# Performance work log

Measured on AMD Instinct MI355X. Metric: run time of the kernel, lower is better.

## Reference

```python
import jax, jax.numpy as jnp
import numpy as np

LN_EPS = 1e-5
OPM_EPS = 1e-3


def setup_inputs() -> dict:
    key = jax.random.key(0)
    ks = jax.random.split(key, 8)
    S, N, c_m, c_h, c_z = 128, 256, 256, 32, 128
    m = jax.random.normal(ks[0], (S, N, c_m), dtype=jnp.float32)
    mask = jnp.ones((S, N), dtype=jnp.float32)
    ln_w = jnp.ones((c_m,), dtype=jnp.float32)
    ln_b = jnp.zeros((c_m,), dtype=jnp.float32)
    sc1 = 1.0 / np.sqrt(c_m)
    w1 = jax.random.uniform(ks[1], (c_m, c_h), jnp.float32, -sc1, sc1)
    b1 = jax.random.uniform(ks[2], (c_h,), jnp.float32, -sc1, sc1)
    w2 = jax.random.uniform(ks[3], (c_m, c_h), jnp.float32, -sc1, sc1)
    b2 = jax.random.uniform(ks[4], (c_h,), jnp.float32, -sc1, sc1)
    sco = 1.0 / np.sqrt(c_h * c_h)
    wo = jax.random.uniform(ks[5], (c_h * c_h, c_z), jnp.float32, -sco, sco)
    bo = jax.random.uniform(ks[6], (c_z,), jnp.float32, -sco, sco)
    return {"m": m, "mask": mask, "ln_w": ln_w, "ln_b": ln_b,
            "w1": w1, "b1": b1, "w2": w2, "b2": b2, "wo": wo, "bo": bo}


def reference(m, mask, ln_w, ln_b, w1, b1, w2, b2, wo, bo):
    # LayerNorm over c_m
    mu = jnp.mean(m, axis=-1, keepdims=True)
    var = jnp.var(m, axis=-1, keepdims=True)
    ln = (m - mu) * jax.lax.rsqrt(var + LN_EPS) * ln_w + ln_b
    mk = mask[..., None]                       # [S, N, 1]
    a = (ln @ w1 + b1) * mk                    # [S, N, c_h]
    b = (ln @ w2 + b2) * mk                    # [S, N, c_h]
    # outer-product mean over the MSA dim s: [N, N, c_h, c_h]
    S, N, ch = a.shape
    outer = jnp.einsum('sic,sjd->ijcd', a, b).reshape(N, N, ch * ch)
    outer = outer @ wo + bo                    # [N, N, c_z]
    norm = jnp.einsum('si,sj->ij', mask, mask)[..., None] + OPM_EPS
    return outer / norm
```

## Files before the change

kernel.cpp:

```cpp
#include <hip/hip_runtime.h>
#include <hip/hip_bf16.h>

typedef __attribute__((ext_vector_type(8))) short short8;
typedef __attribute__((ext_vector_type(4))) short short4v;
typedef __attribute__((ext_vector_type(4))) float float4v;

#define S_DIM 128
#define N_DIM 256
#define CM    256
#define CH    32
#define CZ    128

static __device__ __forceinline__ short f2bf(float v) {
    return __builtin_bit_cast(short, __float2bfloat16(v));
}

__global__ __launch_bounds__(256) void prep_aux_kernel(
    const float* __restrict__ m, const float* __restrict__ mask,
    const float* __restrict__ lnw, const float* __restrict__ lnb,
    const float* __restrict__ w1, const float* __restrict__ b1,
    const float* __restrict__ w2, const float* __restrict__ b2,
    const float* __restrict__ wo, const float* __restrict__ bo,
    __hip_bfloat16* __restrict__ a_t, __hip_bfloat16* __restrict__ b_t,
    __hip_bfloat16* __restrict__ wo_f, float* __restrict__ ninv)
{
    __shared__ __align__(16) char lds_raw[101376];
    __hip_bfloat16* ln_lds = (__hip_bfloat16*)lds_raw;
    __hip_bfloat16* w_lds  = (__hip_bfloat16*)(lds_raw + 67584);
    __hip_bfloat16* st_lds = (__hip_bfloat16*)lds_raw;

    const int bid = blockIdx.x, t = threadIdx.x;

    if (bid >= 320) {
        int i0 = (bid - 320) * 4, j = t;
        float a0 = 0.f, a1 = 0.f, a2 = 0.f, a3 = 0.f;
        for (int s = 0; s < S_DIM; ++s) {
            float mj = mask[s * N_DIM + j];
            a0 += mask[s * N_DIM + i0 + 0] * mj;
            a1 += mask[s * N_DIM + i0 + 1] * mj;
            a2 += mask[s * N_DIM + i0 + 2] * mj;
            a3 += mask[s * N_DIM + i0 + 3] * mj;
        }
        ninv[(i0 + 0) * N_DIM + j] = 1.0f / (a0 + 1e-3f);
        ninv[(i0 + 1) * N_DIM + j] = 1.0f / (a1 + 1e-3f);
        ninv[(i0 + 2) * N_DIM + j] = 1.0f / (a2 + 1e-3f);
        ninv[(i0 + 3) * N_DIM + j] = 1.0f / (a3 + 1e-3f);
        return;
    }
    if (bid >= 256) {
        int fidx = (bid - 256) * 256 + t;
        int l  = fidx & 63;
        int d  = (fidx >> 6) & 31;
        int zt = fidx >> 11;
        int z  = zt * 16 + (l & 15);
        int cb = (l >> 4) * 8;
        short8 frag;
        #pragma unroll
        for (int j = 0; j < 8; ++j)
            frag[j] = f2bf(wo[(size_t)((cb + j) * 32 + d) * CZ + z]);
        *(short8*)&wo_f[(size_t)fidx * 8] = frag;
        return;
    }

    const int lane = t & 63, wv = t >> 6;
    const int q = lane >> 4, c16 = lane & 15;
    const int n0 = (bid & 63) * 4, s0 = (bid >> 6) * 32;

    #pragma unroll 4
    for (int i = 0; i < 64; ++i) {
        int e = i * 256 + t;
        int k = e >> 6, c = e & 63;
        float v = (c < CH) ? w1[k * CH + c] : w2[k * CH + (c - CH)];
        w_lds[c * 264 + k] = __float2bfloat16(v);
    }

    float4 lw = ((const float4*)lnw)[lane];
    float4 lb = ((const float4*)lnb)[lane];

    #pragma unroll 2
    for (int it = 0; it < 32; ++it) {
        int rl = wv * 32 + it;
        int r  = (s0 + (rl >> 2)) * N_DIM + n0 + (rl & 3);
        float4 mv = ((const float4*)(m + (size_t)r * CM))[lane];
        float s1 = mv.x + mv.y + mv.z + mv.w;
        float s2 = mv.x*mv.x + mv.y*mv.y + mv.z*mv.z + mv.w*mv.w;
        #pragma unroll
        for (int o = 32; o > 0; o >>= 1) {
            s1 += __shfl_xor(s1, o, 64);
            s2 += __shfl_xor(s2, o, 64);
        }
        float mu  = s1 * (1.0f / 256.0f);
        float var = s2 * (1.0f / 256.0f) - mu * mu;
        float rs  = rsqrtf(var + 1e-5f);
        int base = rl * 264 + lane * 4;
        ln_lds[base + 0] = __float2bfloat16((mv.x - mu) * rs * lw.x + lb.x);
        ln_lds[base + 1] = __float2bfloat16((mv.y - mu) * rs * lw.y + lb.y);
        ln_lds[base + 2] = __float2bfloat16((mv.z - mu) * rs * lw.z + lb.z);
        ln_lds[base + 3] = __float2bfloat16((mv.w - mu) * rs * lw.w + lb.w);
    }
    __syncthreads();

    float4v acc[2][4];
    #pragma unroll
    for (int rt = 0; rt < 2; ++rt)
        #pragma unroll
        for (int ct = 0; ct < 4; ++ct)
            acc[rt][ct] = (float4v){0.f, 0.f, 0.f, 0.f};
    #pragma unroll
    for (int ks = 0; ks < 8; ++ks) {
        int k0 = ks * 32 + q * 8;
        short8 af0 = *(const short8*)&ln_lds[(wv * 32      + c16) * 264 + k0];
        short8 af1 = *(const short8*)&ln_lds[(wv * 32 + 16 + c16) * 264 + k0];
        #pragma unroll
        for (int ct = 0; ct < 4; ++ct) {
            short8 wb = *(const short8*)&w_lds[(ct * 16 + c16) * 264 + k0];
            acc[0][ct] = __builtin_amdgcn_mfma_f32_16x16x32_bf16(af0, wb, acc[0][ct], 0, 0, 0);
            acc[1][ct] = __builtin_amdgcn_mfma_f32_16x16x32_bf16(af1, wb, acc[1][ct], 0, 0, 0);
        }
    }
    __syncthreads();

    #pragma unroll
    for (int rt = 0; rt < 2; ++rt) {
        int sl = wv * 8 + rt * 4 + q;
        #pragma unroll
        for (int ct = 0; ct < 4; ++ct) {
            int cc = ct * 16 + c16;
            float bias = (cc < CH) ? b1[cc] : b2[cc - CH];
            #pragma unroll
            for (int rr = 0; rr < 4; ++rr) {
                int r = (s0 + sl) * N_DIM + n0 + rr;
                float val = (acc[rt][ct][rr] + bias) * mask[r];
                st_lds[(rr * 64 + cc) * 40 + sl] = __float2bfloat16(val);
            }
        }
    }
    __syncthreads();

    {
        int nl = t >> 6, cc = t & 63;
        int colg = (n0 + nl) * CH + (cc < CH ? cc : cc - CH);
        __hip_bfloat16* dst = (cc < CH ? a_t : b_t) + (size_t)colg * S_DIM + s0;
        #pragma unroll
        for (int v = 0; v < 4; ++v)
            *(short8*)(dst + v * 8) = *(const short8*)&st_lds[t * 40 + v * 8];
    }
}

__global__ __launch_bounds__(512, 4) void main_kernel(
    const __hip_bfloat16* __restrict__ a_t, const __hip_bfloat16* __restrict__ b_t,
    const __hip_bfloat16* __restrict__ wo_f, const float* __restrict__ bo,
    const float* __restrict__ ninv, float* __restrict__ out)
{
    __shared__ __align__(16) short lds[33280];

    const int t = threadIdx.x, l = t & 63, wv = t >> 6;
    const int q = l >> 4, c16 = l & 15;
    const int bi = blockIdx.x, bj0 = blockIdx.y * 2;
    const int wr = wv & 3, wc = wv >> 2;
    const size_t Ibase = (size_t)bi * 128;

    short8 af[4][2];
    #pragma unroll
    for (int sk = 0; sk < 4; ++sk) {
        int koff = sk * 32 + q * 8;
        #pragma unroll
        for (int ti = 0; ti < 2; ++ti) {
            int row = wr * 32 + ti * 16 + c16;
            af[sk][ti] = *(const short8*)&a_t[(Ibase + row) * S_DIM + koff];
        }
    }

    #pragma unroll
    for (int tau = 0; tau < 2; ++tau) {
        const size_t Jbase = (size_t)(bj0 + tau) * 128;
        float4v acc[2][4];
        #pragma unroll
        for (int ti = 0; ti < 2; ++ti)
            #pragma unroll
            for (int tj = 0; tj < 4; ++tj)
                acc[ti][tj] = (float4v){0.f, 0.f, 0.f, 0.f};

        #pragma unroll
        for (int st = 0; st < 2; ++st) {
            #pragma unroll
            for (int i = 0; i < 2; ++i) {
                int f  = i * 8 + wv;
                int h  = f >> 3, ti = (f >> 1) & 3, kk = f & 1;
                int row  = h * 64 + ti * 16 + c16;
                int koff = st * 64 + kk * 32 + q * 8;
                *(short8*)&lds[f * 512 + l * 8] =
                    *(const short8*)&b_t[(Jbase + row) * S_DIM + koff];
            }
            __syncthreads();
            #pragma unroll
            for (int kk = 0; kk < 2; ++kk) {
                short8 bf[4];
                #pragma unroll
                for (int tj = 0; tj < 4; ++tj)
                    bf[tj] = *(const short8*)&lds[((wc * 4 + tj) * 2 + kk) * 512 + l * 8];
                #pragma unroll
                for (int ti = 0; ti < 2; ++ti)
                    #pragma unroll
                    for (int tj = 0; tj < 4; ++tj)
                        acc[ti][tj] = __builtin_amdgcn_mfma_f32_16x16x32_bf16(
                            af[st * 2 + kk][ti], bf[tj], acc[ti][tj], 0, 0, 0);
            }
            __syncthreads();
        }

        const int pb = tau ? 0 : 16640;
        #pragma unroll
        for (int ti = 0; ti < 2; ++ti)
            #pragma unroll
            for (int tj = 0; tj < 4; ++tj) {
                int d  = ((tj & 1) * 16) + c16;
                int c0 = ti * 16 + q * 4;
                int p  = wr * 4 + wc * 2 + (tj >> 1);
                short4v pk;
                #pragma unroll
                for (int rr = 0; rr < 4; ++rr)
                    pk[rr] = f2bf(acc[ti][tj][rr]);
                *(short4v*)&lds[pb + d * 520 + (c0 >> 3) * 128 + p * 8 + (c0 & 7)] = pk;
            }
    }
    __syncthreads();

    float4v oacc[2];
    oacc[0] = (float4v){0.f, 0.f, 0.f, 0.f};
    oacc[1] = (float4v){0.f, 0.f, 0.f, 0.f};
    const __hip_bfloat16* wbase = wo_f + (size_t)wv * 32 * 512;
    #pragma unroll 4
    for (int d = 0; d < 32; ++d) {
        short8 p0 = *(const short8*)&lds[16640 + d * 520 + l * 8];
        short8 p1 = *(const short8*)&lds[        d * 520 + l * 8];
        short8 wf = *(const short8*)&wbase[(size_t)(d * 512 + l * 8)];
        oacc[0] = __builtin_amdgcn_mfma_f32_16x16x32_bf16(p0, wf, oacc[0], 0, 0, 0);
        oacc[1] = __builtin_amdgcn_mfma_f32_16x16x32_bf16(p1, wf, oacc[1], 0, 0, 0);
    }

    const int gi = bi * 4 + q;
    const int z  = wv * 16 + c16;
    const float bz = bo[z];
    #pragma unroll
    for (int tau = 0; tau < 2; ++tau) {
        const int bj = bj0 + tau;
        #pragma unroll
        for (int rr = 0; rr < 4; ++rr) {
            int gj = bj * 4 + rr;
            float nv = ninv[gi * N_DIM + gj];
            out[((size_t)gi * N_DIM + gj) * CZ + z] = (oacc[tau][rr] + bz) * nv;
        }
    }
}

extern "C" void kernel_launch(void* const* d_in, const int* in_sizes, int n_in,
                              void* d_out, int out_size, void* d_ws, size_t ws_size,
                              hipStream_t stream) {
    const float* m    = (const float*)d_in[0];
    const float* mask = (const float*)d_in[1];
    const float* lnw  = (const float*)d_in[2];
    const float* lnb  = (const float*)d_in[3];
    const float* w1   = (const float*)d_in[4];
    const float* b1   = (const float*)d_in[5];
    const float* w2   = (const float*)d_in[6];
    const float* b2   = (const float*)d_in[7];
    const float* wo   = (const float*)d_in[8];
    const float* bo   = (const float*)d_in[9];
    float* out = (float*)d_out;

    char* ws = (char*)d_ws;
    __hip_bfloat16* a_t  = (__hip_bfloat16*)ws;
    __hip_bfloat16* b_t  = (__hip_bfloat16*)(ws + (2u << 20));
    __hip_bfloat16* wo_f = (__hip_bfloat16*)(ws + (4u << 20));
    float*          ninv = (float*)(ws + (4u << 20) + (256u << 10));

    prep_aux_kernel<<<384, 256, 0, stream>>>(m, mask, lnw, lnb, w1, b1, w2, b2,
                                             wo, bo, a_t, b_t, wo_f, ninv);
    main_kernel<<<dim3(64, 32), 512, 0, stream>>>(a_t, b_t, wo_f, bo, ninv, out);
}
```

Baseline: 169.3 us.

## Store a/b projections in MFMA fragment layout and prefetch wo fragments

The prep kernel now handles 2 residues per block (twice as many blocks, smaller LDS footprint) and writes the a/b projections directly in the per-lane MFMA fragment order. The main kernel can then load A and B operands as contiguous 1KB fragments instead of strided row gathers. The final wo projection loop now double-buffers wo fragments in registers to overlap global loads with MFMAs. Risks include extra register pressure in the main kernel and more, smaller prep blocks that re-stage the w1/w2 weights into LDS more often.

```diff
diff --git a/kernel.cpp b/kernel.cpp
--- a/kernel.cpp
+++ b/kernel.cpp
@@ -14,6 +14,7 @@
 static __device__ __forceinline__ short f2bf(float v) {
     return __builtin_bit_cast(short, __float2bfloat16(v));
 }
+
 
 __global__ __launch_bounds__(256) void prep_aux_kernel(
     const float* __restrict__ m, const float* __restrict__ mask,
@@ -21,18 +22,18 @@
     const float* __restrict__ w1, const float* __restrict__ b1,
     const float* __restrict__ w2, const float* __restrict__ b2,
     const float* __restrict__ wo, const float* __restrict__ bo,
-    __hip_bfloat16* __restrict__ a_t, __hip_bfloat16* __restrict__ b_t,
+    __hip_bfloat16* __restrict__ a_f, __hip_bfloat16* __restrict__ b_f,
     __hip_bfloat16* __restrict__ wo_f, float* __restrict__ ninv)
 {
-    __shared__ __align__(16) char lds_raw[101376];
+    __shared__ __align__(16) char lds_raw[77824];
     __hip_bfloat16* ln_lds = (__hip_bfloat16*)lds_raw;
-    __hip_bfloat16* w_lds  = (__hip_bfloat16*)(lds_raw + 67584);
-    __hip_bfloat16* st_lds = (__hip_bfloat16*)lds_raw;
+    __hip_bfloat16* w_lds  = (__hip_bfloat16*)(lds_raw + 33792);
+    __hip_bfloat16* st_lds = (__hip_bfloat16*)(lds_raw + 67584);
 
     const int bid = blockIdx.x, t = threadIdx.x;
 
-    if (bid >= 320) {
-        int i0 = (bid - 320) * 4, j = t;
+    if (bid >= 576) {
+        int i0 = (bid - 576) * 4, j = t;
         float a0 = 0.f, a1 = 0.f, a2 = 0.f, a3 = 0.f;
         for (int s = 0; s < S_DIM; ++s) {
             float mj = mask[s * N_DIM + j];
@@ -47,8 +48,8 @@
         ninv[(i0 + 3) * N_DIM + j] = 1.0f / (a3 + 1e-3f);
         return;
     }
-    if (bid >= 256) {
-        int fidx = (bid - 256) * 256 + t;
+    if (bid >= 512) {
+        int fidx = (bid - 512) * 256 + t;
         int l  = fidx & 63;
         int d  = (fidx >> 6) & 31;
         int zt = fidx >> 11;
@@ -64,7 +65,7 @@
 
     const int lane = t & 63, wv = t >> 6;
     const int q = lane >> 4, c16 = lane & 15;
-    const int n0 = (bid & 63) * 4, s0 = (bid >> 6) * 32;
+    const int n0 = (bid & 127) * 2, s0 = (bid >> 7) * 32, sk = bid >> 7;
 
     #pragma unroll 4
     for (int i = 0; i < 64; ++i) {
@@ -78,9 +79,9 @@
     float4 lb = ((const float4*)lnb)[lane];
 
     #pragma unroll 2
-    for (int it = 0; it < 32; ++it) {
-        int rl = wv * 32 + it;
-        int r  = (s0 + (rl >> 2)) * N_DIM + n0 + (rl & 3);
+    for (int it = 0; it < 16; ++it) {
+        int rl = wv * 16 + it;
+        int r  = (s0 + (rl >> 1)) * N_DIM + n0 + (rl & 1);
         float4 mv = ((const float4*)(m + (size_t)r * CM))[lane];
         float s1 = mv.x + mv.y + mv.z + mv.w;
         float s2 = mv.x*mv.x + mv.y*mv.y + mv.z*mv.z + mv.w*mv.w;
@@ -100,55 +101,49 @@
     }
     __syncthreads();
 
-    float4v acc[2][4];
-    #pragma unroll
-    for (int rt = 0; rt < 2; ++rt)
-        #pragma unroll
-        for (int ct = 0; ct < 4; ++ct)
-            acc[rt][ct] = (float4v){0.f, 0.f, 0.f, 0.f};
+    float4v acc[4];
+    #pragma unroll
+    for (int ct = 0; ct < 4; ++ct) acc[ct] = (float4v){0.f, 0.f, 0.f, 0.f};
     #pragma unroll
     for (int ks = 0; ks < 8; ++ks) {
         int k0 = ks * 32 + q * 8;
-        short8 af0 = *(const short8*)&ln_lds[(wv * 32      + c16) * 264 + k0];
-        short8 af1 = *(const short8*)&ln_lds[(wv * 32 + 16 + c16) * 264 + k0];
+        short8 af = *(const short8*)&ln_lds[(wv * 16 + c16) * 264 + k0];
         #pragma unroll
         for (int ct = 0; ct < 4; ++ct) {
             short8 wb = *(const short8*)&w_lds[(ct * 16 + c16) * 264 + k0];
-            acc[0][ct] = __builtin_amdgcn_mfma_f32_16x16x32_bf16(af0, wb, acc[0][ct], 0, 0, 0);
-            acc[1][ct] = __builtin_amdgcn_mfma_f32_16x16x32_bf16(af1, wb, acc[1][ct], 0, 0, 0);
+            acc[ct] = __builtin_amdgcn_mfma_f32_16x16x32_bf16(af, wb, acc[ct], 0, 0, 0);
+        }
+    }
+
+    #pragma unroll
+    for (int ct = 0; ct < 4; ++ct) {
+        int cc = ct * 16 + c16;
+        float bias = (cc < CH) ? b1[cc] : b2[cc - CH];
+        #pragma unroll
+        for (int rr = 0; rr < 4; ++rr) {
+            int rl = wv * 16 + q * 4 + rr;
+            int r  = (s0 + (rl >> 1)) * N_DIM + n0 + (rl & 1);
+            float val = (acc[ct][rr] + bias) * mask[r];
+            st_lds[((rl & 1) * 64 + cc) * 40 + (rl >> 1)] = __float2bfloat16(val);
         }
     }
     __syncthreads();
 
     #pragma unroll
-    for (int rt = 0; rt < 2; ++rt) {
-        int sl = wv * 8 + rt * 4 + q;
-        #pragma unroll
-        for (int ct = 0; ct < 4; ++ct) {
-            int cc = ct * 16 + c16;
-            float bias = (cc < CH) ? b1[cc] : b2[cc - CH];
-            #pragma unroll
-            for (int rr = 0; rr < 4; ++rr) {
-                int r = (s0 + sl) * N_DIM + n0 + rr;
-                float val = (acc[rt][ct][rr] + bias) * mask[r];
-                st_lds[(rr * 64 + cc) * 40 + sl] = __float2bfloat16(val);
-            }
-        }
-    }
-    __syncthreads();
-
-    {
-        int nl = t >> 6, cc = t & 63;
-        int colg = (n0 + nl) * CH + (cc < CH ? cc : cc - CH);
-        __hip_bfloat16* dst = (cc < CH ? a_t : b_t) + (size_t)colg * S_DIM + s0;
-        #pragma unroll
-        for (int v = 0; v < 4; ++v)
-            *(short8*)(dst + v * 8) = *(const short8*)&st_lds[t * 40 + v * 8];
+    for (int i = 0; i < 2; ++i) {
+        int slot = i * 256 + t;
+        int f8 = slot >> 6, l = slot & 63;
+        int fl = f8 & 3, nl = fl >> 1, cch = fl & 1;
+        int lq = l >> 4, lc16 = l & 15;
+        int col = nl * 64 + (f8 >= 4 ? 32 : 0) + cch * 16 + lc16;
+        short8 v = *(const short8*)&st_lds[col * 40 + lq * 8];
+        __hip_bfloat16* base = (f8 >= 4) ? b_f : a_f;
+        *(short8*)&base[(size_t)((n0 * 2 + fl) * 4 + sk) * 512 + l * 8] = v;
     }
 }
 
 __global__ __launch_bounds__(512, 4) void main_kernel(
-    const __hip_bfloat16* __restrict__ a_t, const __hip_bfloat16* __restrict__ b_t,
+    const __hip_bfloat16* __restrict__ a_f, const __hip_bfloat16* __restrict__ b_f,
     const __hip_bfloat16* __restrict__ wo_f, const float* __restrict__ bo,
     const float* __restrict__ ninv, float* __restrict__ out)
 {
@@ -158,22 +153,18 @@
     const int q = l >> 4, c16 = l & 15;
     const int bi = blockIdx.x, bj0 = blockIdx.y * 2;
     const int wr = wv & 3, wc = wv >> 2;
-    const size_t Ibase = (size_t)bi * 128;
+    const size_t Ix = (size_t)bi * 8;
 
     short8 af[4][2];
     #pragma unroll
-    for (int sk = 0; sk < 4; ++sk) {
-        int koff = sk * 32 + q * 8;
-        #pragma unroll
-        for (int ti = 0; ti < 2; ++ti) {
-            int row = wr * 32 + ti * 16 + c16;
-            af[sk][ti] = *(const short8*)&a_t[(Ibase + row) * S_DIM + koff];
-        }
-    }
+    for (int sk = 0; sk < 4; ++sk)
+        #pragma unroll
+        for (int ti = 0; ti < 2; ++ti)
+            af[sk][ti] = *(const short8*)&a_f[((Ix + wr * 2 + ti) * 4 + sk) * 512 + l * 8];
 
     #pragma unroll
     for (int tau = 0; tau < 2; ++tau) {
-        const size_t Jbase = (size_t)(bj0 + tau) * 128;
+        const size_t Jx = (size_t)(bj0 + tau) * 8;
         float4v acc[2][4];
         #pragma unroll
         for (int ti = 0; ti < 2; ++ti)
@@ -186,11 +177,9 @@
             #pragma unroll
             for (int i = 0; i < 2; ++i) {
                 int f  = i * 8 + wv;
-                int h  = f >> 3, ti = (f >> 1) & 3, kk = f & 1;
-                int row  = h * 64 + ti * 16 + c16;
-                int koff = st * 64 + kk * 32 + q * 8;
+                int xl = f >> 1, kk = f & 1;
                 *(short8*)&lds[f * 512 + l * 8] =
-                    *(const short8*)&b_t[(Jbase + row) * S_DIM + koff];
+                    *(const short8*)&b_f[((Jx + xl) * 4 + st * 2 + kk) * 512 + l * 8];
             }
             __syncthreads();
             #pragma unroll
@@ -230,13 +219,27 @@
     oacc[0] = (float4v){0.f, 0.f, 0.f, 0.f};
     oacc[1] = (float4v){0.f, 0.f, 0.f, 0.f};
     const __hip_bfloat16* wbase = wo_f + (size_t)wv * 32 * 512;
-    #pragma unroll 4
-    for (int d = 0; d < 32; ++d) {
-        short8 p0 = *(const short8*)&lds[16640 + d * 520 + l * 8];
-        short8 p1 = *(const short8*)&lds[        d * 520 + l * 8];
-        short8 wf = *(const short8*)&wbase[(size_t)(d * 512 + l * 8)];
-        oacc[0] = __builtin_amdgcn_mfma_f32_16x16x32_bf16(p0, wf, oacc[0], 0, 0, 0);
-        oacc[1] = __builtin_amdgcn_mfma_f32_16x16x32_bf16(p1, wf, oacc[1], 0, 0, 0);
+    short8 wA[4], wB[4];
+    #pragma unroll
+    for (int dd = 0; dd < 4; ++dd) {
+        wA[dd] = *(const short8*)&wbase[(dd    ) * 512 + l * 8];
+        wB[dd] = *(const short8*)&wbase[(dd + 4) * 512 + l * 8];
+    }
+    #pragma unroll
+    for (int c = 0; c < 8; ++c) {
+        #pragma unroll
+        for (int dd = 0; dd < 4; ++dd) {
+            int d = c * 4 + dd;
+            short8 wf = (c & 1) ? wB[dd] : wA[dd];
+            short8 p0 = *(const short8*)&lds[16640 + d * 520 + l * 8];
+            short8 p1 = *(const short8*)&lds[        d * 520 + l * 8];
+            if (c < 6) {
+                short8 wn = *(const short8*)&wbase[(d + 8) * 512 + l * 8];
+                if (c & 1) wB[dd] = wn; else wA[dd] = wn;
+            }
+            oacc[0] = __builtin_amdgcn_mfma_f32_16x16x32_bf16(p0, wf, oacc[0], 0, 0, 0);
+            oacc[1] = __builtin_amdgcn_mfma_f32_16x16x32_bf16(p1, wf, oacc[1], 0, 0, 0);
+        }
     }
 
     const int gi = bi * 4 + q;
@@ -270,12 +273,12 @@
     float* out = (float*)d_out;
 
     char* ws = (char*)d_ws;
-    __hip_bfloat16* a_t  = (__hip_bfloat16*)ws;
-    __hip_bfloat16* b_t  = (__hip_bfloat16*)(ws + (2u << 20));
+    __hip_bfloat16* a_f  = (__hip_bfloat16*)ws;
+    __hip_bfloat16* b_f  = (__hip_bfloat16*)(ws + (2u << 20));
     __hip_bfloat16* wo_f = (__hip_bfloat16*)(ws + (4u << 20));
     float*          ninv = (float*)(ws + (4u << 20) + (256u << 10));
 
-    prep_aux_kernel<<<384, 256, 0, stream>>>(m, mask, lnw, lnb, w1, b1, w2, b2,
-                                             wo, bo, a_t, b_t, wo_f, ninv);
-    main_kernel<<<dim3(64, 32), 512, 0, stream>>>(a_t, b_t, wo_f, bo, ninv, out);
-}
+    prep_aux_kernel<<<640, 256, 0, stream>>>(m, mask, lnw, lnb, w1, b1, w2, b2,
+                                             wo, bo, a_f, b_f, wo_f, ninv);
+    main_kernel<<<dim3(64, 32), 512, 0, stream>>>(a_f, b_f, wo_f, bo, ninv, out);
+}
```

After: 147.1 us. -13.2%, faster.
